# Kernel tuning notes

Measured on AMD Instinct MI355X. Metric: run time of the kernel, lower is better.

Reference implementation:

```python
import jax, jax.numpy as jnp
import numpy as np

TMPL = jnp.array([[-0.9, 1.2, 0.0], [0.0, 0.0, 0.0], [2.5, 0.0, 0.0]], dtype=jnp.float32)
EYE3 = jnp.eye(3, dtype=jnp.float32)


def _normalize(v, eps=1e-12):
    n = jnp.maximum(jnp.linalg.norm(v, axis=-1, keepdims=True), eps)
    return v / n


def _layer_norm(x, g, b, eps=1e-5):
    mu = jnp.mean(x, axis=-1, keepdims=True)
    var = jnp.var(x, axis=-1, keepdims=True)
    return (x - mu) * jax.lax.rsqrt(var + eps) * g + b


def _build_frames(coords, mask):
    P = coords[..., 0, :]
    C4p = coords[..., 1, :]
    N = coords[..., 2, :]
    e1 = _normalize(N - C4p)
    u = P - C4p
    e2 = _normalize(u - jnp.sum(u * e1, axis=-1, keepdims=True) * e1)
    e3 = jnp.cross(e1, e2)
    R = jnp.stack([e1, e2, e3], axis=-1)  # (B,L,3,3), columns = e1,e2,e3
    pad = ~mask
    R = jnp.where(pad[..., None, None], EYE3, R)
    return R, C4p


def _invariants(R, t):
    # dt[b,i,j] = t[b,j] - t[b,i]
    dt = t[:, None, :, :] - t[:, :, None, :]  # (B,L,L,3)
    # local frame of i: Ri^T @ dt
    dt_l = jnp.einsum('bixk,bijx->bijk', R, dt)  # (B,L,L,3)
    dist = jnp.maximum(jnp.linalg.norm(dt, axis=-1, keepdims=True), 1e-4)
    log_d = jnp.log(dist)
    # trace(Ri^T Rj)
    trace = jnp.einsum('bixk,bjxk->bij', R, R)[..., None]  # (B,L,L,1)
    cos_a = jnp.clip((trace - 1.0) / 2.0, -1.0, 1.0)
    return jnp.concatenate([dist, dt_l, trace, cos_a, log_d], axis=-1)  # (B,L,L,7)


def _skew(v):
    z = jnp.zeros_like(v[..., 0])
    x, y, zz = v[..., 0], v[..., 1], v[..., 2]
    r0 = jnp.stack([z, -zz, y], axis=-1)
    r1 = jnp.stack([zz, z, -x], axis=-1)
    r2 = jnp.stack([-y, x, z], axis=-1)
    return jnp.stack([r0, r1, r2], axis=-2)


def _apply_frame_update(R, t, dr, dt, mask):
    mf = mask.astype(R.dtype)[..., None]
    dr = dr * mf
    dt = dt * mf
    angle = jnp.maximum(jnp.linalg.norm(dr, axis=-1, keepdims=True), 1e-8)
    axis = dr / angle
    cos_a = jnp.cos(angle)[..., None]
    sin_a = jnp.sin(angle)[..., None]
    K = _skew(axis)
    outer = axis[..., :, None] * axis[..., None, :]
    R_delta = cos_a * EYE3 + sin_a * K + (1.0 - cos_a) * outer
    R_new = R_delta @ R
    t_new = t + jnp.einsum('blxy,bly->blx', R, dt)
    return R_new, t_new


def _reconstruct_atoms(R, t):
    # coords[b,l,a,:] = t[b,l] + R[b,l] @ TMPL[a]
    d = jnp.einsum('blxy,ay->blax', R, TMPL)
    return t[:, :, None, :] + d


def _gelu(x):
    return jax.nn.gelu(x, approximate=False)


def _forward(h, coords, mask, pair_w1, pair_b1, pair_w2, pair_b2, gw_w, gw_b, ga_w, ga_b,
             ln_g, ln_b, fh_ln_g, fh_ln_b, fh_w1, fh_b1, fh_w2, fh_b2):
    R, t = _build_frames(coords, mask)
    n_steps = pair_w1.shape[0]
    coords_list = []
    for s in range(n_steps):
        inv = _invariants(R, t)  # (B,L,L,7)
        pm = (mask[:, None, :] & mask[:, :, None]).astype(h.dtype)  # (B,L,L)
        msg = _gelu(inv @ pair_w1[s] + pair_b1[s]) @ pair_w2[s] + pair_b2[s]  # (B,L,L,D)
        n_v = jnp.maximum(jnp.sum(pm, axis=2, keepdims=True), 1.0)  # (B,L,1)
        agg = jnp.sum(msg * pm[..., None], axis=2) / n_v  # (B,L,D)
        h_s = _layer_norm(h, ln_g[s], ln_b[s])
        cat = jnp.concatenate([h_s, agg], axis=-1)
        g = cat @ gw_w[s] + gw_b[s]
        a = jax.nn.sigmoid(cat @ ga_w[s] + ga_b[s])
        h_aug = h + a * g
        fh = _gelu(_layer_norm(h_aug, fh_ln_g, fh_ln_b) @ fh_w1 + fh_b1) @ fh_w2 + fh_b2
        delta_r, delta_t = fh[..., :3], fh[..., 3:]
        R, t = _apply_frame_update(R, t, delta_r, delta_t, mask)
        coords_list.append(_reconstruct_atoms(R, t))
    return coords_list[-1], jnp.stack(coords_list, axis=0)


def setup_inputs() -> dict:
    key = jax.random.key(0)
    B, L, D, H, S = 2, 512, 256, 64, 4
    ks = jax.random.split(key, 16)
    w = lambda k, shp: jax.random.normal(k, shp, dtype=jnp.float32) * 0.02
    return {
        'h': jax.random.normal(ks[0], (B, L, D), dtype=jnp.float32),
        'coords': jax.random.normal(ks[1], (B, L, 3, 3), dtype=jnp.float32),
        'mask': jnp.ones((B, L), dtype=bool),
        'pair_w1': w(ks[2], (S, 7, H)), 'pair_b1': jnp.zeros((S, H), jnp.float32),
        'pair_w2': w(ks[3], (S, H, D)), 'pair_b2': jnp.zeros((S, D), jnp.float32),
        'gw_w': w(ks[4], (S, 2 * D, D)), 'gw_b': jnp.zeros((S, D), jnp.float32),
        'ga_w': w(ks[5], (S, 2 * D, D)), 'ga_b': jnp.zeros((S, D), jnp.float32),
        'ln_g': jnp.ones((S, D), jnp.float32), 'ln_b': jnp.zeros((S, D), jnp.float32),
        'fh_ln_g': jnp.ones((D,), jnp.float32), 'fh_ln_b': jnp.zeros((D,), jnp.float32),
        'fh_w1': w(ks[6], (D, D // 2)), 'fh_b1': jnp.zeros((D // 2,), jnp.float32),
        'fh_w2': w(ks[7], (D // 2, 6)), 'fh_b2': jnp.zeros((6,), jnp.float32),
    }


def reference(h, coords, mask, pair_w1, pair_b1, pair_w2, pair_b2, gw_w, gw_b, ga_w, ga_b,
              ln_g, ln_b, fh_ln_g, fh_ln_b, fh_w1, fh_b1, fh_w2, fh_b2):
    return _forward(h, coords, mask, pair_w1, pair_b1, pair_w2, pair_b2, gw_w, gw_b,
                    ga_w, ga_b, ln_g, ln_b, fh_ln_g, fh_ln_b, fh_w1, fh_b1, fh_w2, fh_b2)
```

## Files before the change

kernel.cpp:

```cpp
#include <hip/hip_runtime.h>
#include <math.h>

#define BB 2
#define LL 512
#define DD 256
#define HH 64
#define NSTEP 4
#define NTOK (BB * LL)

__device__ __forceinline__ float geluf(float x) {
    return 0.5f * x * (1.0f + erff(x * 0.70710678118654752f));
}
__device__ __forceinline__ float sigmoidf_(float x) {
    return 1.0f / (1.0f + expf(-x));
}
__device__ __forceinline__ float gelu_fast(float x) {
    float u = 0.70710678118654752f * x;
    float a = fabsf(u);
    float t = __builtin_amdgcn_rcpf(fmaf(0.3275911f, a, 1.0f));
    float p = fmaf(t, 1.061405429f, -1.453152027f);
    p = fmaf(t, p, 1.421413741f);
    p = fmaf(t, p, -0.284496736f);
    p = fmaf(t, p, 0.254829592f);
    p = p * t;
    float e = __expf(-u * u);
    float erfa = fmaf(-p, e, 1.0f);
    float erfu = copysignf(erfa, u);
    return 0.5f * x * (1.0f + erfu);
}
__device__ __forceinline__ float rlane(float v, int l) {
    return __int_as_float(__builtin_amdgcn_readlane(__float_as_int(v), l));
}
#define F4C(v, j) ((j) == 0 ? (v).x : (j) == 1 ? (v).y : (j) == 2 ? (v).z : (v).w)

__global__ void build_frames_kernel(const float* __restrict__ coords,
                                    float* __restrict__ Rg, float* __restrict__ tg) {
    int idx = blockIdx.x * blockDim.x + threadIdx.x;
    if (idx >= NTOK) return;
    const float* c = coords + idx * 9;
    float Px = c[0], Py = c[1], Pz = c[2];
    float Cx = c[3], Cy = c[4], Cz = c[5];
    float Nx = c[6], Ny = c[7], Nz = c[8];
    float e1x = Nx - Cx, e1y = Ny - Cy, e1z = Nz - Cz;
    float n1 = fmaxf(sqrtf(e1x * e1x + e1y * e1y + e1z * e1z), 1e-12f);
    e1x /= n1; e1y /= n1; e1z /= n1;
    float ux = Px - Cx, uy = Py - Cy, uz = Pz - Cz;
    float du = ux * e1x + uy * e1y + uz * e1z;
    float e2x = ux - du * e1x, e2y = uy - du * e1y, e2z = uz - du * e1z;
    float n2 = fmaxf(sqrtf(e2x * e2x + e2y * e2y + e2z * e2z), 1e-12f);
    e2x /= n2; e2y /= n2; e2z /= n2;
    float e3x = e1y * e2z - e1z * e2y;
    float e3y = e1z * e2x - e1x * e2z;
    float e3z = e1x * e2y - e1y * e2x;
    float* Rp = Rg + idx * 9;
    Rp[0] = e1x; Rp[1] = e2x; Rp[2] = e3x;
    Rp[3] = e1y; Rp[4] = e2y; Rp[5] = e3y;
    Rp[6] = e1z; Rp[7] = e2z; Rp[8] = e3z;
    tg[idx * 3 + 0] = Cx; tg[idx * 3 + 1] = Cy; tg[idx * 3 + 2] = Cz;
}

__global__ __launch_bounds__(256) void ln4_kernel(
        const float* __restrict__ hIn,
        const float* __restrict__ lng, const float* __restrict__ lnb,
        float* __restrict__ hln) {
    __shared__ float redsh[8];
    const int i = blockIdx.x;
    const int tid = threadIdx.x;
    const int wv = tid >> 6, lane = tid & 63;
    float hv = hIn[(size_t)i * DD + tid];
    float s1 = hv, s2 = hv * hv;
#pragma unroll
    for (int off = 32; off > 0; off >>= 1) {
        s1 += __shfl_xor(s1, off);
        s2 += __shfl_xor(s2, off);
    }
    if (lane == 0) { redsh[wv * 2] = s1; redsh[wv * 2 + 1] = s2; }
    __syncthreads();
    float S1 = redsh[0] + redsh[2] + redsh[4] + redsh[6];
    float S2 = redsh[1] + redsh[3] + redsh[5] + redsh[7];
    float mu = S1 * (1.0f / DD);
    float var = S2 * (1.0f / DD) - mu * mu;
    float rs = rsqrtf(var + 1e-5f);
    float hn = (hv - mu) * rs;
#pragma unroll
    for (int s = 0; s < NSTEP; s++)
        hln[((size_t)s * NTOK + i) * DD + tid] = hn * lng[s * DD + tid] + lnb[s * DD + tid];
}

__global__ __launch_bounds__(256) void fuse_w_kernel(
        const float* __restrict__ w2all, const float* __restrict__ b2all,
        const float* __restrict__ gww, const float* __restrict__ gaw,
        const float* __restrict__ gwb, const float* __restrict__ gab,
        float* __restrict__ Wfus, float* __restrict__ biasGA) {
    __shared__ float bsh[256 * 17];

    const int bid = blockIdx.x;
    const int s = bid >> 5;
    const int gate = (bid >> 4) & 1;
    const int ct = bid & 15;
    const int c0 = ct * 16;
    const int tid = threadIdx.x;

    const float* Wb = (gate ? gaw : gww) + (size_t)s * 2 * DD * DD + (size_t)DD * DD;
    {
        const float* src = Wb + (size_t)tid * DD + c0;
        float4 a0 = *(const float4*)(src + 0);
        float4 a1 = *(const float4*)(src + 4);
        float4 a2 = *(const float4*)(src + 8);
        float4 a3 = *(const float4*)(src + 12);
        float* dst = &bsh[tid * 17];
        dst[0] = a0.x; dst[1] = a0.y; dst[2] = a0.z; dst[3] = a0.w;
        dst[4] = a1.x; dst[5] = a1.y; dst[6] = a1.z; dst[7] = a1.w;
        dst[8] = a2.x; dst[9] = a2.y; dst[10] = a2.z; dst[11] = a2.w;
        dst[12] = a3.x; dst[13] = a3.y; dst[14] = a3.z; dst[15] = a3.w;
    }
    __syncthreads();

    const int r = tid & 63;
    const int cg = tid >> 6;
    const float* w2p = w2all + (size_t)s * HH * DD + (size_t)r * DD;
    float4 acc = {0.f, 0.f, 0.f, 0.f};
#pragma unroll 4
    for (int k4 = 0; k4 < 64; k4++) {
        float4 wv = *(const float4*)(w2p + k4 * 4);
#pragma unroll
        for (int j = 0; j < 4; j++) {
            const float* bp = &bsh[(k4 * 4 + j) * 17 + cg * 4];
            float w = F4C(wv, j);
            acc.x = fmaf(w, bp[0], acc.x);
            acc.y = fmaf(w, bp[1], acc.y);
            acc.z = fmaf(w, bp[2], acc.z);
            acc.w = fmaf(w, bp[3], acc.w);
        }
    }
    acc.x *= (1.0f / 512.0f); acc.y *= (1.0f / 512.0f);
    acc.z *= (1.0f / 512.0f); acc.w *= (1.0f / 512.0f);
    *(float4*)&Wfus[((size_t)s * HH + r) * 512 + gate * 256 + c0 + cg * 4] = acc;

    if (tid < 16) {
        const float* b2 = b2all + s * DD;
        float a = 0.0f;
#pragma unroll 4
        for (int m = 0; m < 256; m++) a = fmaf(b2[m], bsh[m * 17 + tid], a);
        const float* gb = (gate ? gab : gwb) + s * DD;
        biasGA[(size_t)s * 512 + gate * 256 + c0 + tid] = a + gb[c0 + tid];
    }
}

__global__ __launch_bounds__(256) void gpreh_kernel(
        const float* __restrict__ hln,
        const float* __restrict__ gww, const float* __restrict__ gaw,
        const float* __restrict__ biasGA,
        float* __restrict__ gpreH) {
    __shared__ float hsh[16 * DD];
    const int bid = blockIdx.x;
    const int s = bid >> 7;
    const int gate = (bid >> 6) & 1;
    const int mt = bid & 63;
    const int tid = threadIdx.x;

    const float* hsrc = hln + ((size_t)s * NTOK + mt * 16) * DD;
    for (int k = tid; k < 16 * DD; k += 256) hsh[k] = hsrc[k];
    __syncthreads();

    const float* W = (gate ? gaw : gww) + (size_t)s * 2 * DD * DD;
    float bias = biasGA[(size_t)s * 512 + gate * 256 + tid];
    float acc[16];
#pragma unroll
    for (int t = 0; t < 16; t++) acc[t] = bias;
#pragma unroll 4
    for (int k = 0; k < DD; k++) {
        float w = W[(size_t)k * DD + tid];
#pragma unroll
        for (int t = 0; t < 16; t++) acc[t] = fmaf(hsh[t * DD + k], w, acc[t]);
    }
    float* out = gpreH + ((size_t)s * NTOK + mt * 16) * 512 + gate * 256 + tid;
#pragma unroll
    for (int t = 0; t < 16; t++) out[(size_t)t * 512] = acc[t];
}

__global__ __launch_bounds__(256) void mega_kernel(
        const float* __restrict__ Rin, const float* __restrict__ tin,
        float* __restrict__ Rout, float* __restrict__ tout,
        const float* __restrict__ w1, const float* __restrict__ b1,
        const float* __restrict__ WfusS, const float* __restrict__ gpreHS,
        const float* __restrict__ hIn,
        const float* __restrict__ fhlng, const float* __restrict__ fhlnb,
        const float* __restrict__ fhw1, const float* __restrict__ fhb1,
        const float* __restrict__ fhw2, const float* __restrict__ fhb2,
        float* __restrict__ outFinal, float* __restrict__ outStack, int s) {
    __shared__ float Rsh[LL * 9];
    __shared__ float tsh[LL * 3];
    __shared__ float accbuf[256];
    __shared__ float asum[HH];
    __shared__ float ln2s[DD];
    __shared__ float fh1p[2 * 128];
    __shared__ float fh1s[128];
    __shared__ float partS[24];
    __shared__ float fhsh[6];
    __shared__ float redsh[8];

    const int i = blockIdx.x;
    const int b = i >> 9;
    const int l = i & (LL - 1);
    const int tid = threadIdx.x;
    const int g = tid >> 6;
    const int hh = tid & 63;

    const float* Rb = Rin + (size_t)b * LL * 9;
    const float* tb = tin + (size_t)b * LL * 3;
    for (int k = tid; k < LL * 9; k += 256) Rsh[k] = Rb[k];
    for (int k = tid; k < LL * 3; k += 256) tsh[k] = tb[k];
    __syncthreads();

    float Ri[9];
#pragma unroll
    for (int k = 0; k < 9; k++) Ri[k] = Rsh[l * 9 + k];
    const float tix = tsh[l * 3 + 0], tiy = tsh[l * 3 + 1], tiz = tsh[l * 3 + 2];

    const float w0 = w1[0 * HH + hh];
    const float wA = w1[1 * HH + hh];
    const float wB = w1[2 * HH + hh];
    const float wC = w1[3 * HH + hh];
    const float w5 = w1[5 * HH + hh];
    const float w4 = fmaf(0.5f, w5, w1[4 * HH + hh]);
    const float w6 = w1[6 * HH + hh];
    const float b1r = fmaf(-0.5f, w5, b1[hh]);

    float acc = 0.0f;
#pragma unroll
    for (int jc = 0; jc < 2; jc++) {
        const int j = jc * 256 + g * 64 + hh;
        float dx = tsh[j * 3 + 0] - tix;
        float dy = tsh[j * 3 + 1] - tiy;
        float dz = tsh[j * 3 + 2] - tiz;
        float dl0 = Ri[0] * dx + Ri[3] * dy + Ri[6] * dz;
        float dl1 = Ri[1] * dx + Ri[4] * dy + Ri[7] * dz;
        float dl2 = Ri[2] * dx + Ri[5] * dy + Ri[8] * dz;
        float dist = fmaxf(sqrtf(dx * dx + dy * dy + dz * dz), 1e-4f);
        float tr = 0.0f;
#pragma unroll
        for (int k = 0; k < 9; k++) tr = fmaf(Ri[k], Rsh[j * 9 + k], tr);
        float lgd = logf(dist);
#pragma unroll
        for (int jj = 0; jj < 64; jj++) {
            float x = b1r;
            x = fmaf(rlane(dist, jj), w0, x);
            x = fmaf(rlane(dl0, jj), wA, x);
            x = fmaf(rlane(dl1, jj), wB, x);
            x = fmaf(rlane(dl2, jj), wC, x);
            x = fmaf(rlane(tr, jj), w4, x);
            x = fmaf(rlane(lgd, jj), w6, x);
            acc += gelu_fast(x);
        }
    }
    accbuf[tid] = acc;
    __syncthreads();
    if (tid < HH)
        asum[tid] = accbuf[tid] + accbuf[64 + tid] + accbuf[128 + tid] + accbuf[192 + tid];
    __syncthreads();

    float gpg = gpreHS[(size_t)i * 512 + tid];
    float gpa = gpreHS[(size_t)i * 512 + 256 + tid];
#pragma unroll 8
    for (int k = 0; k < HH; k++) {
        float av = asum[k];
        gpg = fmaf(av, WfusS[(size_t)k * 512 + tid], gpg);
        gpa = fmaf(av, WfusS[(size_t)k * 512 + 256 + tid], gpa);
    }
    float hv = hIn[(size_t)i * DD + tid];
    float haug = hv + sigmoidf_(gpa) * gpg;

    {
        float s1 = haug, s2 = haug * haug;
#pragma unroll
        for (int off = 32; off > 0; off >>= 1) {
            s1 += __shfl_xor(s1, off);
            s2 += __shfl_xor(s2, off);
        }
        if (hh == 0) { redsh[g * 2] = s1; redsh[g * 2 + 1] = s2; }
    }
    __syncthreads();
    {
        float S1 = redsh[0] + redsh[2] + redsh[4] + redsh[6];
        float S2 = redsh[1] + redsh[3] + redsh[5] + redsh[7];
        float mu = S1 * (1.0f / DD);
        float var = S2 * (1.0f / DD) - mu * mu;
        float rs = rsqrtf(var + 1e-5f);
        ln2s[tid] = (haug - mu) * rs * fhlng[tid] + fhlnb[tid];
    }
    __syncthreads();

    {
        const int col = tid & 127;
        const int kh = tid >> 7;
        float a = 0.0f;
        const float* wp = fhw1 + (size_t)(kh * 128) * 128 + col;
        const float* lp = &ln2s[kh * 128];
#pragma unroll 8
        for (int k = 0; k < 128; k++) a = fmaf(lp[k], wp[(size_t)k * 128], a);
        fh1p[kh * 128 + col] = a;
    }
    __syncthreads();
    if (tid < 128) fh1s[tid] = geluf(fh1p[tid] + fh1p[128 + tid] + fhb1[tid]);
    __syncthreads();

    if (tid < 24) {
        const int kq = tid / 6, m = tid % 6;
        float a = 0.0f;
#pragma unroll
        for (int j = 0; j < 32; j++) {
            int k = kq * 32 + j;
            a = fmaf(fh1s[k], fhw2[k * 6 + m], a);
        }
        partS[tid] = a;
    }
    __syncthreads();
    if (tid < 6)
        fhsh[tid] = partS[tid] + partS[6 + tid] + partS[12 + tid] + partS[18 + tid] + fhb2[tid];
    __syncthreads();

    if (tid == 0) {
        float R9[9], t3[3];
#pragma unroll
        for (int k = 0; k < 9; k++) R9[k] = Rsh[l * 9 + k];
        t3[0] = tix; t3[1] = tiy; t3[2] = tiz;
        float drx = fhsh[0], dry = fhsh[1], drz = fhsh[2];
        float dtx = fhsh[3], dty = fhsh[4], dtz = fhsh[5];
        float ang = fmaxf(sqrtf(drx * drx + dry * dry + drz * drz), 1e-8f);
        float ax = drx / ang, ay = dry / ang, az = drz / ang;
        float ca = cosf(ang), sa = sinf(ang), omc = 1.0f - ca;
        float Rd[9];
        Rd[0] = ca + omc * ax * ax;        Rd[1] = -sa * az + omc * ax * ay;  Rd[2] = sa * ay + omc * ax * az;
        Rd[3] = sa * az + omc * ay * ax;   Rd[4] = ca + omc * ay * ay;        Rd[5] = -sa * ax + omc * ay * az;
        Rd[6] = -sa * ay + omc * az * ax;  Rd[7] = sa * ax + omc * az * ay;   Rd[8] = ca + omc * az * az;
        float Rn[9];
#pragma unroll
        for (int x = 0; x < 3; x++)
#pragma unroll
            for (int y = 0; y < 3; y++)
                Rn[x * 3 + y] = Rd[x * 3 + 0] * R9[0 * 3 + y]
                              + Rd[x * 3 + 1] * R9[1 * 3 + y]
                              + Rd[x * 3 + 2] * R9[2 * 3 + y];
        float tn[3];
#pragma unroll
        for (int x = 0; x < 3; x++)
            tn[x] = t3[x] + R9[x * 3 + 0] * dtx + R9[x * 3 + 1] * dty + R9[x * 3 + 2] * dtz;
#pragma unroll
        for (int k = 0; k < 9; k++) Rout[(size_t)i * 9 + k] = Rn[k];
#pragma unroll
        for (int k = 0; k < 3; k++) tout[(size_t)i * 3 + k] = tn[k];
        float* os = outStack + ((size_t)s * NTOK + i) * 9;
        float av[9];
#pragma unroll
        for (int x = 0; x < 3; x++) {
            float r0 = Rn[x * 3 + 0], r1 = Rn[x * 3 + 1];
            av[0 * 3 + x] = tn[x] - 0.9f * r0 + 1.2f * r1;
            av[1 * 3 + x] = tn[x];
            av[2 * 3 + x] = tn[x] + 2.5f * r0;
        }
#pragma unroll
        for (int k = 0; k < 9; k++) os[k] = av[k];
        if (s == NSTEP - 1) {
            float* of = outFinal + (size_t)i * 9;
#pragma unroll
            for (int k = 0; k < 9; k++) of[k] = av[k];
        }
    }
}

extern "C" void kernel_launch(void* const* d_in, const int* in_sizes, int n_in,
                              void* d_out, int out_size, void* d_ws, size_t ws_size,
                              hipStream_t stream) {
    const float* h      = (const float*)d_in[0];
    const float* coords = (const float*)d_in[1];
    const float* pw1   = (const float*)d_in[3];
    const float* pb1   = (const float*)d_in[4];
    const float* pw2   = (const float*)d_in[5];
    const float* pb2   = (const float*)d_in[6];
    const float* gww   = (const float*)d_in[7];
    const float* gwb   = (const float*)d_in[8];
    const float* gaw   = (const float*)d_in[9];
    const float* gab   = (const float*)d_in[10];
    const float* lng   = (const float*)d_in[11];
    const float* lnb   = (const float*)d_in[12];
    const float* fhlng = (const float*)d_in[13];
    const float* fhlnb = (const float*)d_in[14];
    const float* fhw1  = (const float*)d_in[15];
    const float* fhb1  = (const float*)d_in[16];
    const float* fhw2  = (const float*)d_in[17];
    const float* fhb2  = (const float*)d_in[18];

    float* ws     = (float*)d_ws;
    float* R0     = ws;
    float* t0     = ws + 9216;
    float* R1     = ws + 12288;
    float* t1     = ws + 21504;
    float* hln    = ws + 24576;
    float* gpreH  = ws + 24576 + 1048576;
    float* Wfus   = ws + 24576 + 1048576 + 2097152;
    float* biasGA = ws + 24576 + 1048576 + 2097152 + 131072;

    float* outFinal = (float*)d_out;
    float* outStack = outFinal + NTOK * 9;

    build_frames_kernel<<<NTOK / 256, 256, 0, stream>>>(coords, R0, t0);
    ln4_kernel<<<NTOK, 256, 0, stream>>>(h, lng, lnb, hln);
    fuse_w_kernel<<<128, 256, 0, stream>>>(pw2, pb2, gww, gaw, gwb, gab, Wfus, biasGA);
    gpreh_kernel<<<512, 256, 0, stream>>>(hln, gww, gaw, biasGA, gpreH);

    for (int s = 0; s < NSTEP; s++) {
        const float* Rin = (s & 1) ? R1 : R0;
        const float* tin = (s & 1) ? t1 : t0;
        float* Rout = (s & 1) ? R0 : R1;
        float* tout = (s & 1) ? t0 : t1;
        mega_kernel<<<NTOK, 256, 0, stream>>>(
            Rin, tin, Rout, tout,
            pw1 + s * 7 * HH, pb1 + s * HH,
            Wfus + (size_t)s * HH * 512, gpreH + (size_t)s * NTOK * 512,
            h, fhlng, fhlnb, fhw1, fhb1, fhw2, fhb2,
            outFinal, outStack, s);
    }
}
```

Measured before the change: 218.6 us.

## Split pair-MLP hidden units across waves instead of readlane-broadcasting pair features

Each lane now computes invariant features for 8 residues j and keeps them in registers. Each wave owns 16 hidden units, with weights read as float4 from a transposed LDS table. Per-hidden sums are reduced with xor-shuffles across the wave. This removes the six v_readlane broadcasts per GELU evaluation and the cross-wave LDS accumulation buffer. The cost is that all four waves now compute the full set of pair features (sqrt, log, trace), adding redundant per-pair work, 96 shuffles per thread, and more live registers.

```diff
diff --git a/kernel.cpp b/kernel.cpp
--- a/kernel.cpp
+++ b/kernel.cpp
@@ -27,9 +27,6 @@
     float erfa = fmaf(-p, e, 1.0f);
     float erfu = copysignf(erfa, u);
     return 0.5f * x * (1.0f + erfu);
-}
-__device__ __forceinline__ float rlane(float v, int l) {
-    return __int_as_float(__builtin_amdgcn_readlane(__float_as_int(v), l));
 }
 #define F4C(v, j) ((j) == 0 ? (v).x : (j) == 1 ? (v).y : (j) == 2 ? (v).z : (v).w)
 
@@ -191,7 +188,7 @@
         float* __restrict__ outFinal, float* __restrict__ outStack, int s) {
     __shared__ float Rsh[LL * 9];
     __shared__ float tsh[LL * 3];
-    __shared__ float accbuf[256];
+    __shared__ float w1t[HH * 8];
     __shared__ float asum[HH];
     __shared__ float ln2s[DD];
     __shared__ float fh1p[2 * 128];
@@ -211,6 +208,17 @@
     const float* tb = tin + (size_t)b * LL * 3;
     for (int k = tid; k < LL * 9; k += 256) Rsh[k] = Rb[k];
     for (int k = tid; k < LL * 3; k += 256) tsh[k] = tb[k];
+    if (tid < HH) {
+        float w5 = w1[5 * HH + tid];
+        w1t[tid * 8 + 0] = w1[0 * HH + tid];
+        w1t[tid * 8 + 1] = w1[1 * HH + tid];
+        w1t[tid * 8 + 2] = w1[2 * HH + tid];
+        w1t[tid * 8 + 3] = w1[3 * HH + tid];
+        w1t[tid * 8 + 4] = fmaf(0.5f, w5, w1[4 * HH + tid]);
+        w1t[tid * 8 + 5] = w1[6 * HH + tid];
+        w1t[tid * 8 + 6] = fmaf(-0.5f, w5, b1[tid]);
+        w1t[tid * 8 + 7] = 0.0f;
+    }
     __syncthreads();
 
     float Ri[9];
@@ -218,46 +226,56 @@
     for (int k = 0; k < 9; k++) Ri[k] = Rsh[l * 9 + k];
     const float tix = tsh[l * 3 + 0], tiy = tsh[l * 3 + 1], tiz = tsh[l * 3 + 2];
 
-    const float w0 = w1[0 * HH + hh];
-    const float wA = w1[1 * HH + hh];
-    const float wB = w1[2 * HH + hh];
-    const float wC = w1[3 * HH + hh];
-    const float w5 = w1[5 * HH + hh];
-    const float w4 = fmaf(0.5f, w5, w1[4 * HH + hh]);
-    const float w6 = w1[6 * HH + hh];
-    const float b1r = fmaf(-0.5f, w5, b1[hh]);
-
-    float acc = 0.0f;
-#pragma unroll
-    for (int jc = 0; jc < 2; jc++) {
-        const int j = jc * 256 + g * 64 + hh;
+    float fd[8], f0[8], f1[8], f2[8], ft[8], fl[8];
+#pragma unroll
+    for (int c = 0; c < 8; c++) {
+        const int j = c * 64 + hh;
         float dx = tsh[j * 3 + 0] - tix;
         float dy = tsh[j * 3 + 1] - tiy;
         float dz = tsh[j * 3 + 2] - tiz;
-        float dl0 = Ri[0] * dx + Ri[3] * dy + Ri[6] * dz;
-        float dl1 = Ri[1] * dx + Ri[4] * dy + Ri[7] * dz;
-        float dl2 = Ri[2] * dx + Ri[5] * dy + Ri[8] * dz;
+        f0[c] = Ri[0] * dx + Ri[3] * dy + Ri[6] * dz;
+        f1[c] = Ri[1] * dx + Ri[4] * dy + Ri[7] * dz;
+        f2[c] = Ri[2] * dx + Ri[5] * dy + Ri[8] * dz;
         float dist = fmaxf(sqrtf(dx * dx + dy * dy + dz * dz), 1e-4f);
+        fd[c] = dist;
         float tr = 0.0f;
 #pragma unroll
         for (int k = 0; k < 9; k++) tr = fmaf(Ri[k], Rsh[j * 9 + k], tr);
-        float lgd = logf(dist);
-#pragma unroll
-        for (int jj = 0; jj < 64; jj++) {
-            float x = b1r;
-            x = fmaf(rlane(dist, jj), w0, x);
-            x = fmaf(rlane(dl0, jj), wA, x);
-            x = fmaf(rlane(dl1, jj), wB, x);
-            x = fmaf(rlane(dl2, jj), wC, x);
-            x = fmaf(rlane(tr, jj), w4, x);
-            x = fmaf(rlane(lgd, jj), w6, x);
-            acc += gelu_fast(x);
-        }
-    }
-    accbuf[tid] = acc;
-    __syncthreads();
-    if (tid < HH)
-        asum[tid] = accbuf[tid] + accbuf[64 + tid] + accbuf[128 + tid] + accbuf[192 + tid];
+        ft[c] = tr;
+        fl[c] = logf(dist);
+    }
+
+    const int h0 = g * 16;
+    float acc[16];
+#pragma unroll
+    for (int k = 0; k < 16; k++) acc[k] = 0.0f;
+#pragma unroll
+    for (int k = 0; k < 16; k++) {
+        const float4 wa = *(const float4*)&w1t[(h0 + k) * 8];
+        const float4 wb = *(const float4*)&w1t[(h0 + k) * 8 + 4];
+#pragma unroll
+        for (int c = 0; c < 8; c++) {
+            float x = wb.z;
+            x = fmaf(fd[c], wa.x, x);
+            x = fmaf(f0[c], wa.y, x);
+            x = fmaf(f1[c], wa.z, x);
+            x = fmaf(f2[c], wa.w, x);
+            x = fmaf(ft[c], wb.x, x);
+            x = fmaf(fl[c], wb.y, x);
+            acc[k] += gelu_fast(x);
+        }
+    }
+    {
+        float mine = 0.0f;
+#pragma unroll
+        for (int k = 0; k < 16; k++) {
+            float v = acc[k];
+#pragma unroll
+            for (int off = 1; off < 64; off <<= 1) v += __shfl_xor(v, off);
+            if (hh == k) mine = v;
+        }
+        if (hh < 16) asum[h0 + hh] = mine;
+    }
     __syncthreads();
 
     float gpg = gpreHS[(size_t)i * 512 + tid];
```

Result: no change. 214.8 us (-1.7%).
